# Kernel optimization log

Hardware: AMD Instinct MI355X
Metric: run time of the kernel (lower is better)

Reference implementation:

```python
import jax, jax.numpy as jnp
import numpy as np

K = 10        # neighbors kept (after dropping self)
N_SEEDS = 20  # FPS seeds
H = 0.01      # repulsion bandwidth


def setup_inputs() -> dict:
    key = jax.random.key(0)
    pcs = jax.random.uniform(key, (16, 65536, 3), dtype=jnp.float32)
    return {"pcs": pcs}


def farthest_point_sample(xyz, npoint, key):
    """Iterative FPS. xyz: [B,N,C] -> centroids [B,npoint] (int)."""
    B, N, C = xyz.shape
    distance = jnp.full((B, N), 1e10, dtype=xyz.dtype)
    farthest = jax.random.randint(key, (B,), 0, N)
    bidx = jnp.arange(B)

    def step(carry, _):
        dist_min, far = carry
        centroid = xyz[bidx, far][:, None, :]              # [B,1,C]
        d = jnp.sum((xyz - centroid) ** 2, axis=-1)        # [B,N]
        dist_min = jnp.minimum(dist_min, d)
        return (dist_min, jnp.argmax(dist_min, axis=-1)), far

    _, cents = jax.lax.scan(step, (distance, farthest), None, length=npoint)
    return cents.T  # [B, npoint]


def reference(pcs):
    B, N, C = pcs.shape
    seeds = farthest_point_sample(pcs, N_SEEDS, jax.random.key(1))   # [B,S]
    seeds_value = jnp.take_along_axis(
        pcs, jnp.broadcast_to(seeds[:, :, None], (B, N_SEEDS, C)), axis=1
    )  # [B,S,3]
    diff = pcs[:, :, None, :] - seeds_value[:, None, :, :]           # [B,N,S,3]
    sq = jnp.sum(diff * diff, axis=-1)                               # [B,N,S]
    # safe L2 norm (exact zeros at seed-vs-itself)
    dist = jnp.where(sq == 0, 0.0, jnp.sqrt(jnp.where(sq == 0, 1.0, sq)))
    dist_sn = dist.transpose(0, 2, 1)                                # [B,S,N]
    # k+1 smallest distances per seed, ascending (torch.topk largest=False)
    neg_top, _ = jax.lax.top_k(-dist_sn, K + 1)                      # [B,S,K+1]
    top_dist_net = -neg_top[:, :, 1:]                                # drop self, [B,S,K]
    weights = jnp.exp(-(top_dist_net ** 2) / (H * H))
    repulsion = -top_dist_net * weights
    return repulsion.sum(axis=2).sum(axis=1).mean()
```

## Files before the change

### kernel.cpp

```cpp
#include <hip/hip_runtime.h>
#include <cstdint>
#include <cfloat>
#include <cmath>

#define NPTS 65536
#define NB 16
#define NS 20
#define KK 10
#define FPB 16
#define NSm1 (NS - 1)

struct InitIdx { int idx[NB]; };

static __device__ __forceinline__ unsigned long long
agent_ld(const unsigned long long* p) {
    return __hip_atomic_load(p, __ATOMIC_RELAXED, __HIP_MEMORY_SCOPE_AGENT);
}

__global__ __launch_bounds__(1024) void fps_kernel(const float* __restrict__ pcs,
                                                   int* __restrict__ seeds,
                                                   unsigned long long* __restrict__ fkey,
                                                   InitIdx init) {
    const int u   = blockIdx.x;
    const int xcd = u & 7;
    const int k   = u >> 3;
    const int b   = 2 * xcd + (k >> 4);
    const int j   = k & 15;
    const int t   = threadIdx.x;
    const int lane = t & 63;
    const int w    = t >> 6;
    const float* __restrict__ base = pcs + (size_t)b * NPTS * 3;
    const int pbase = j * 4096 + t * 4;

    const float4* q4 = reinterpret_cast<const float4*>(base + (size_t)pbase * 3);
    float4 A = q4[0], Bv = q4[1], Cv = q4[2];
    float x[4] = { A.x, A.w, Bv.z, Cv.y };
    float y[4] = { A.y, Bv.x, Bv.w, Cv.z };
    float z[4] = { A.z, Bv.y, Cv.x, Cv.w };
    float dm[4] = { 1e10f, 1e10f, 1e10f, 1e10f };

    __shared__ float s_val[16];
    __shared__ int   s_idx[16];
    __shared__ int   s_far;

    int far = init.idx[b];

    for (int s = 0; s < NS; ++s) {
        if (j == 0 && t == 0) seeds[b * NS + s] = far;
        if (s == NSm1) break;

        const float* c = base + (size_t)far * 3;
        const float cx = c[0], cy = c[1], cz = c[2];

        float bestv = -1.0f;
        int   besti = 0;
#pragma unroll
        for (int q = 0; q < 4; ++q) {
            float dx = __fsub_rn(x[q], cx);
            float dy = __fsub_rn(y[q], cy);
            float dz = __fsub_rn(z[q], cz);
            float d  = __fadd_rn(__fadd_rn(__fmul_rn(dx, dx), __fmul_rn(dy, dy)),
                                 __fmul_rn(dz, dz));
            dm[q] = fminf(dm[q], d);
            if (dm[q] > bestv) { bestv = dm[q]; besti = pbase + q; }
        }
#pragma unroll
        for (int off = 32; off >= 1; off >>= 1) {
            float ov = __shfl_down(bestv, off);
            int   oi = __shfl_down(besti, off);
            if (ov > bestv || (ov == bestv && oi < besti)) { bestv = ov; besti = oi; }
        }
        if (lane == 0) { s_val[w] = bestv; s_idx[w] = besti; }
        __syncthreads();

        if (w == 0) {
            unsigned long long kv = 0ULL;
            if (lane < 16) {
                kv = ((unsigned long long)__float_as_uint(s_val[lane]) << 32) |
                     (unsigned long long)(0xFFFFFFFFu - (unsigned int)s_idx[lane]);
            }
#pragma unroll
            for (int off = 8; off >= 1; off >>= 1) {
                unsigned int lo = (unsigned int)kv, hi = (unsigned int)(kv >> 32);
                unsigned int olo = (unsigned int)__shfl_xor((int)lo, off);
                unsigned int ohi = (unsigned int)__shfl_xor((int)hi, off);
                unsigned long long o = ((unsigned long long)ohi << 32) | olo;
                if (o > kv) kv = o;
            }
            unsigned long long* fp = fkey + (size_t)(b * NS + s) * FPB;
            if (lane == 0)
                __hip_atomic_store(&fp[j], kv, __ATOMIC_RELAXED,
                                   __HIP_MEMORY_SCOPE_AGENT);

            const unsigned long long* sl = fp + (lane & 15);
            unsigned long long p0 = agent_ld(sl);
            unsigned long long p1 = agent_ld(sl);
            unsigned long long p2 = agent_ld(sl);
            unsigned long long v;
            for (;;) {
                if (!__any(p0 == 0ULL)) { v = p0; break; }
                p0 = agent_ld(sl);
                if (!__any(p1 == 0ULL)) { v = p1; break; }
                p1 = agent_ld(sl);
                if (!__any(p2 == 0ULL)) { v = p2; break; }
                p2 = agent_ld(sl);
            }
#pragma unroll
            for (int off = 32; off >= 1; off >>= 1) {
                unsigned int lo = (unsigned int)v, hi = (unsigned int)(v >> 32);
                unsigned int olo = (unsigned int)__shfl_xor((int)lo, off);
                unsigned int ohi = (unsigned int)__shfl_xor((int)hi, off);
                unsigned long long o = ((unsigned long long)ohi << 32) | olo;
                if (o > v) v = o;
            }
            if (lane == 0)
                s_far = (int)(0xFFFFFFFFu - (unsigned int)(v & 0xFFFFFFFFull));
        }
        __syncthreads();
        far = s_far;
    }
}

__global__ __launch_bounds__(1024) void knn_kernel(const float* __restrict__ pcs,
                                                   const int* __restrict__ seeds,
                                                   float* __restrict__ out) {
    const int u   = blockIdx.x;
    const int xcd = u & 7;
    const int k   = u >> 3;
    const int b   = 2 * xcd + (k & 1);
    const int s   = k >> 1;
    const int t = threadIdx.x;
    const int lane = t & 63;
    const int w = t >> 6;
    const float* __restrict__ base = pcs + (size_t)b * NPTS * 3;
    const int sidx = seeds[b * NS + s];
    const float cx = base[(size_t)sidx * 3 + 0];
    const float cy = base[(size_t)sidx * 3 + 1];
    const float cz = base[(size_t)sidx * 3 + 2];

    float lst[11];
#pragma unroll
    for (int jj = 0; jj < 11; ++jj) lst[jj] = FLT_MAX;

    for (int i = 0; i < 16; ++i) {
        const int pbase = i * 4096 + t * 4;
        const float4* q4 = reinterpret_cast<const float4*>(base + (size_t)pbase * 3);
        float4 A = q4[0], Bv = q4[1], Cv = q4[2];
        float px[4] = { A.x, A.w, Bv.z, Cv.y };
        float py[4] = { A.y, Bv.x, Bv.w, Cv.z };
        float pz[4] = { A.z, Bv.y, Cv.x, Cv.w };
#pragma unroll
        for (int q = 0; q < 4; ++q) {
            float dx = __fsub_rn(px[q], cx);
            float dy = __fsub_rn(py[q], cy);
            float dz = __fsub_rn(pz[q], cz);
            float sq = __fadd_rn(__fadd_rn(__fmul_rn(dx, dx), __fmul_rn(dy, dy)),
                                 __fmul_rn(dz, dz));
#pragma unroll
            for (int jj = 10; jj >= 1; --jj)
                lst[jj] = __builtin_amdgcn_fmed3f(lst[jj - 1], lst[jj], sq);
            lst[0] = fminf(lst[0], sq);
        }
    }

    __shared__ float s_top[16][11];
    for (int r = 0; r < 11; ++r) {
        float v = lst[0];
#pragma unroll
        for (int off = 32; off >= 1; off >>= 1) v = fminf(v, __shfl_xor(v, off));
        unsigned long long m = __ballot(lst[0] == v);
        if (lane == (int)__ffsll(m) - 1) {
#pragma unroll
            for (int jj = 0; jj < 10; ++jj) lst[jj] = lst[jj + 1];
            lst[10] = FLT_MAX;
        }
        if (lane == 0) s_top[w][r] = v;
    }
    __syncthreads();

    if (w == 0) {
        const float* flat = &s_top[0][0];
        float a0 = flat[lane];
        float a1 = flat[lane + 64];
        float a2 = (lane + 128 < 176) ? flat[lane + 128] : FLT_MAX;

        const float HH = (float)(0.01 * 0.01);
        float acc = 0.0f;
#pragma unroll
        for (int r = 0; r < 11; ++r) {
            float mymin = fminf(a0, fminf(a1, a2));
            float v = mymin;
#pragma unroll
            for (int off = 32; off >= 1; off >>= 1) v = fminf(v, __shfl_xor(v, off));
            unsigned long long m = __ballot(mymin == v);
            if (lane == (int)__ffsll(m) - 1) {
                if (a0 == v)      a0 = FLT_MAX;
                else if (a1 == v) a1 = FLT_MAX;
                else              a2 = FLT_MAX;
            }
            if (lane == 0 && r >= 1) {
                float sq = v;
                float d  = (sq == 0.0f) ? 0.0f : __fsqrt_rn(sq);
                float q2 = __fmul_rn(d, d);
                float wt = expf(__fdiv_rn(-q2, HH));
                acc = __fadd_rn(acc, -__fmul_rn(d, wt));
            }
        }
        if (lane == 0) atomicAdd(out, acc * 0.0625f);
    }
}

static inline uint32_t rotl32(uint32_t x, uint32_t d) { return (x << d) | (x >> (32 - d)); }

static void tf2x32(uint32_t k0, uint32_t k1, uint32_t x0, uint32_t x1,
                   uint32_t& y0, uint32_t& y1) {
    const uint32_t ks[3] = { k0, k1, k0 ^ k1 ^ 0x1BD11BDAu };
    const uint32_t rotA[4] = { 13, 15, 26, 6 };
    const uint32_t rotB[4] = { 17, 29, 16, 24 };
    uint32_t v0 = x0 + ks[0], v1 = x1 + ks[1];
    for (int i = 0; i < 5; ++i) {
        const uint32_t* rot = (i % 2 == 0) ? rotA : rotB;
        for (int j = 0; j < 4; ++j) {
            v0 += v1;
            v1 = rotl32(v1, rot[j]);
            v1 ^= v0;
        }
        v0 += ks[(i + 1) % 3];
        v1 += ks[(i + 2) % 3] + (uint32_t)(i + 1);
    }
    y0 = v0; y1 = v1;
}

extern "C" void kernel_launch(void* const* d_in, const int* in_sizes, int n_in,
                              void* d_out, int out_size, void* d_ws, size_t ws_size,
                              hipStream_t stream) {
    const float* pcs = (const float*)d_in[0];
    float* out = (float*)d_out;

    int* seeds               = (int*)d_ws;
    unsigned long long* fkey = (unsigned long long*)((char*)d_ws + 2048);

    uint32_t k2_0, k2_1;
    tf2x32(0u, 1u, 0u, 1u, k2_0, k2_1);
    InitIdx init;
    for (int i = 0; i < NB; ++i) {
        uint32_t y0, y1;
        tf2x32(k2_0, k2_1, 0u, (uint32_t)i, y0, y1);
        init.idx[i] = (int)((y0 ^ y1) & 0xFFFFu);
    }

    hipMemsetAsync(d_ws, 0, 43008, stream);
    hipMemsetAsync(d_out, 0, sizeof(float), stream);

    hipLaunchKernelGGL(fps_kernel, dim3(NB * FPB), dim3(1024), 0, stream,
                       pcs, seeds, fkey, init);
    hipLaunchKernelGGL(knn_kernel, dim3(NB * NS), dim3(1024), 0, stream,
                       pcs, seeds, out);
}
```

Measured before the change: 82.35 us.

## Halve FPS blocks per batch and split KNN scan into smaller blocks with merge kernel

```diff
diff --git a/kernel.cpp b/kernel.cpp
--- a/kernel.cpp
+++ b/kernel.cpp
@@ -7,7 +7,8 @@
 #define NB 16
 #define NS 20
 #define KK 10
-#define FPB 16
+#define FPB 8
+#define PPT 8
 #define NSm1 (NS - 1)
 
 struct InitIdx { int idx[NB]; };
@@ -24,20 +25,28 @@
     const int u   = blockIdx.x;
     const int xcd = u & 7;
     const int k   = u >> 3;
-    const int b   = 2 * xcd + (k >> 4);
-    const int j   = k & 15;
+    const int b   = 2 * xcd + (k >> 3);
+    const int j   = k & 7;
     const int t   = threadIdx.x;
     const int lane = t & 63;
     const int w    = t >> 6;
     const float* __restrict__ base = pcs + (size_t)b * NPTS * 3;
-    const int pbase = j * 4096 + t * 4;
-
-    const float4* q4 = reinterpret_cast<const float4*>(base + (size_t)pbase * 3);
-    float4 A = q4[0], Bv = q4[1], Cv = q4[2];
-    float x[4] = { A.x, A.w, Bv.z, Cv.y };
-    float y[4] = { A.y, Bv.x, Bv.w, Cv.z };
-    float z[4] = { A.z, Bv.y, Cv.x, Cv.w };
-    float dm[4] = { 1e10f, 1e10f, 1e10f, 1e10f };
+    const int pbase = j * 8192 + t * 8;
+
+    float x[PPT], y[PPT], z[PPT], dm[PPT];
+    {
+        const float4* q4 = reinterpret_cast<const float4*>(base + (size_t)pbase * 3);
+#pragma unroll
+        for (int g = 0; g < 2; ++g) {
+            float4 A = q4[g * 3 + 0], Bv = q4[g * 3 + 1], Cv = q4[g * 3 + 2];
+            x[g*4+0] = A.x;  y[g*4+0] = A.y;  z[g*4+0] = A.z;
+            x[g*4+1] = A.w;  y[g*4+1] = Bv.x; z[g*4+1] = Bv.y;
+            x[g*4+2] = Bv.z; y[g*4+2] = Bv.w; z[g*4+2] = Cv.x;
+            x[g*4+3] = Cv.y; y[g*4+3] = Cv.z; z[g*4+3] = Cv.w;
+        }
+#pragma unroll
+        for (int q = 0; q < PPT; ++q) dm[q] = 1e10f;
+    }
 
     __shared__ float s_val[16];
     __shared__ int   s_idx[16];
@@ -55,7 +64,7 @@
         float bestv = -1.0f;
         int   besti = 0;
 #pragma unroll
-        for (int q = 0; q < 4; ++q) {
+        for (int q = 0; q < PPT; ++q) {
             float dx = __fsub_rn(x[q], cx);
             float dy = __fsub_rn(y[q], cy);
             float dz = __fsub_rn(z[q], cz);
@@ -92,7 +101,7 @@
                 __hip_atomic_store(&fp[j], kv, __ATOMIC_RELAXED,
                                    __HIP_MEMORY_SCOPE_AGENT);
 
-            const unsigned long long* sl = fp + (lane & 15);
+            const unsigned long long* sl = fp + (lane & 7);
             unsigned long long p0 = agent_ld(sl);
             unsigned long long p1 = agent_ld(sl);
             unsigned long long p2 = agent_ld(sl);
@@ -121,14 +130,16 @@
     }
 }
 
-__global__ __launch_bounds__(1024) void knn_kernel(const float* __restrict__ pcs,
-                                                   const int* __restrict__ seeds,
-                                                   float* __restrict__ out) {
+__global__ __launch_bounds__(256) void knn_scan(const float* __restrict__ pcs,
+                                                const int* __restrict__ seeds,
+                                                float* __restrict__ part) {
     const int u   = blockIdx.x;
     const int xcd = u & 7;
     const int k   = u >> 3;
-    const int b   = 2 * xcd + (k & 1);
-    const int s   = k >> 1;
+    const int b   = 2 * xcd + (k / 80);
+    const int rem = k % 80;
+    const int s   = rem >> 2;
+    const int c   = rem & 3;
     const int t = threadIdx.x;
     const int lane = t & 63;
     const int w = t >> 6;
@@ -143,7 +154,7 @@
     for (int jj = 0; jj < 11; ++jj) lst[jj] = FLT_MAX;
 
     for (int i = 0; i < 16; ++i) {
-        const int pbase = i * 4096 + t * 4;
+        const int pbase = c * 16384 + i * 1024 + t * 4;
         const float4* q4 = reinterpret_cast<const float4*>(base + (size_t)pbase * 3);
         float4 A = q4[0], Bv = q4[1], Cv = q4[2];
         float px[4] = { A.x, A.w, Bv.z, Cv.y };
@@ -163,7 +174,7 @@
         }
     }
 
-    __shared__ float s_top[16][11];
+    float* pr = part + ((size_t)((b * NS + s) * 4 + c) * 4 + w) * 11;
     for (int r = 0; r < 11; ++r) {
         float v = lst[0];
 #pragma unroll
@@ -174,40 +185,42 @@
             for (int jj = 0; jj < 10; ++jj) lst[jj] = lst[jj + 1];
             lst[10] = FLT_MAX;
         }
-        if (lane == 0) s_top[w][r] = v;
-    }
-    __syncthreads();
-
-    if (w == 0) {
-        const float* flat = &s_top[0][0];
-        float a0 = flat[lane];
-        float a1 = flat[lane + 64];
-        float a2 = (lane + 128 < 176) ? flat[lane + 128] : FLT_MAX;
-
-        const float HH = (float)(0.01 * 0.01);
-        float acc = 0.0f;
-#pragma unroll
-        for (int r = 0; r < 11; ++r) {
-            float mymin = fminf(a0, fminf(a1, a2));
-            float v = mymin;
-#pragma unroll
-            for (int off = 32; off >= 1; off >>= 1) v = fminf(v, __shfl_xor(v, off));
-            unsigned long long m = __ballot(mymin == v);
-            if (lane == (int)__ffsll(m) - 1) {
-                if (a0 == v)      a0 = FLT_MAX;
-                else if (a1 == v) a1 = FLT_MAX;
-                else              a2 = FLT_MAX;
-            }
-            if (lane == 0 && r >= 1) {
-                float sq = v;
-                float d  = (sq == 0.0f) ? 0.0f : __fsqrt_rn(sq);
-                float q2 = __fmul_rn(d, d);
-                float wt = expf(__fdiv_rn(-q2, HH));
-                acc = __fadd_rn(acc, -__fmul_rn(d, wt));
-            }
-        }
-        if (lane == 0) atomicAdd(out, acc * 0.0625f);
-    }
+        if (lane == 0) pr[r] = v;
+    }
+}
+
+__global__ __launch_bounds__(64) void knn_merge(const float* __restrict__ part,
+                                                float* __restrict__ out) {
+    const int pair = blockIdx.x;
+    const int lane = threadIdx.x;
+    const float* flat = part + (size_t)pair * 176;
+    float a0 = flat[lane];
+    float a1 = flat[lane + 64];
+    float a2 = (lane + 128 < 176) ? flat[lane + 128] : FLT_MAX;
+
+    const float HH = (float)(0.01 * 0.01);
+    float acc = 0.0f;
+#pragma unroll
+    for (int r = 0; r < 11; ++r) {
+        float mymin = fminf(a0, fminf(a1, a2));
+        float v = mymin;
+#pragma unroll
+        for (int off = 32; off >= 1; off >>= 1) v = fminf(v, __shfl_xor(v, off));
+        unsigned long long m = __ballot(mymin == v);
+        if (lane == (int)__ffsll(m) - 1) {
+            if (a0 == v)      a0 = FLT_MAX;
+            else if (a1 == v) a1 = FLT_MAX;
+            else              a2 = FLT_MAX;
+        }
+        if (lane == 0 && r >= 1) {
+            float sq = v;
+            float d  = (sq == 0.0f) ? 0.0f : __fsqrt_rn(sq);
+            float q2 = __fmul_rn(d, d);
+            float wt = expf(__fdiv_rn(-q2, HH));
+            acc = __fadd_rn(acc, -__fmul_rn(d, wt));
+        }
+    }
+    if (lane == 0) atomicAdd(out, acc * 0.0625f);
 }
 
 static inline uint32_t rotl32(uint32_t x, uint32_t d) { return (x << d) | (x >> (32 - d)); }
@@ -239,6 +252,7 @@
 
     int* seeds               = (int*)d_ws;
     unsigned long long* fkey = (unsigned long long*)((char*)d_ws + 2048);
+    float* part              = (float*)((char*)d_ws + 24576);
 
     uint32_t k2_0, k2_1;
     tf2x32(0u, 1u, 0u, 1u, k2_0, k2_1);
@@ -249,11 +263,13 @@
         init.idx[i] = (int)((y0 ^ y1) & 0xFFFFu);
     }
 
-    hipMemsetAsync(d_ws, 0, 43008, stream);
+    hipMemsetAsync(d_ws, 0, 22528, stream);
     hipMemsetAsync(d_out, 0, sizeof(float), stream);
 
     hipLaunchKernelGGL(fps_kernel, dim3(NB * FPB), dim3(1024), 0, stream,
                        pcs, seeds, fkey, init);
-    hipLaunchKernelGGL(knn_kernel, dim3(NB * NS), dim3(1024), 0, stream,
-                       pcs, seeds, out);
-}
+    hipLaunchKernelGGL(knn_scan, dim3(1280), dim3(256), 0, stream,
+                       pcs, seeds, part);
+    hipLaunchKernelGGL(knn_merge, dim3(320), dim3(64), 0, stream,
+                       part, out);
+}
```

After: 81.83 us. Within noise of the previous version (-0.6%).

## Split kNN into chunked multi-seed scan and separate merge kernel

Applied to the files above, without the earlier changes.

```diff
diff --git a/kernel.cpp b/kernel.cpp
--- a/kernel.cpp
+++ b/kernel.cpp
@@ -9,6 +9,9 @@
 #define KK 10
 #define FPB 16
 #define NSm1 (NS - 1)
+#define NCH 8
+#define NSG 4
+#define SPG 5
 
 struct InitIdx { int idx[NB]; };
 
@@ -121,29 +124,38 @@
     }
 }
 
-__global__ __launch_bounds__(1024) void knn_kernel(const float* __restrict__ pcs,
-                                                   const int* __restrict__ seeds,
-                                                   float* __restrict__ out) {
+__global__ __launch_bounds__(256) void knn_scan(const float* __restrict__ pcs,
+                                                const int* __restrict__ seeds,
+                                                float* __restrict__ part) {
     const int u   = blockIdx.x;
     const int xcd = u & 7;
     const int k   = u >> 3;
-    const int b   = 2 * xcd + (k & 1);
-    const int s   = k >> 1;
+    const int b   = 2 * xcd + (k >> 5);
+    const int rem = k & 31;
+    const int ch  = rem >> 2;
+    const int sg  = rem & 3;
     const int t = threadIdx.x;
     const int lane = t & 63;
     const int w = t >> 6;
     const float* __restrict__ base = pcs + (size_t)b * NPTS * 3;
-    const int sidx = seeds[b * NS + s];
-    const float cx = base[(size_t)sidx * 3 + 0];
-    const float cy = base[(size_t)sidx * 3 + 1];
-    const float cz = base[(size_t)sidx * 3 + 2];
-
-    float lst[11];
-#pragma unroll
-    for (int jj = 0; jj < 11; ++jj) lst[jj] = FLT_MAX;
-
-    for (int i = 0; i < 16; ++i) {
-        const int pbase = i * 4096 + t * 4;
+
+    float scx[SPG], scy[SPG], scz[SPG];
+#pragma unroll
+    for (int g = 0; g < SPG; ++g) {
+        const int sidx = seeds[b * NS + sg * SPG + g];
+        scx[g] = base[(size_t)sidx * 3 + 0];
+        scy[g] = base[(size_t)sidx * 3 + 1];
+        scz[g] = base[(size_t)sidx * 3 + 2];
+    }
+
+    float lst[SPG][11];
+#pragma unroll
+    for (int g = 0; g < SPG; ++g)
+#pragma unroll
+        for (int jj = 0; jj < 11; ++jj) lst[g][jj] = FLT_MAX;
+
+    for (int i = 0; i < 8; ++i) {
+        const int pbase = ch * 8192 + i * 1024 + t * 4;
         const float4* q4 = reinterpret_cast<const float4*>(base + (size_t)pbase * 3);
         float4 A = q4[0], Bv = q4[1], Cv = q4[2];
         float px[4] = { A.x, A.w, Bv.z, Cv.y };
@@ -151,63 +163,80 @@
         float pz[4] = { A.z, Bv.y, Cv.x, Cv.w };
 #pragma unroll
         for (int q = 0; q < 4; ++q) {
-            float dx = __fsub_rn(px[q], cx);
-            float dy = __fsub_rn(py[q], cy);
-            float dz = __fsub_rn(pz[q], cz);
-            float sq = __fadd_rn(__fadd_rn(__fmul_rn(dx, dx), __fmul_rn(dy, dy)),
-                                 __fmul_rn(dz, dz));
-#pragma unroll
-            for (int jj = 10; jj >= 1; --jj)
-                lst[jj] = __builtin_amdgcn_fmed3f(lst[jj - 1], lst[jj], sq);
-            lst[0] = fminf(lst[0], sq);
-        }
-    }
-
-    __shared__ float s_top[16][11];
+#pragma unroll
+            for (int g = 0; g < SPG; ++g) {
+                float dx = __fsub_rn(px[q], scx[g]);
+                float dy = __fsub_rn(py[q], scy[g]);
+                float dz = __fsub_rn(pz[q], scz[g]);
+                float sq = __fadd_rn(__fadd_rn(__fmul_rn(dx, dx),
+                                               __fmul_rn(dy, dy)),
+                                     __fmul_rn(dz, dz));
+#pragma unroll
+                for (int jj = 10; jj >= 1; --jj)
+                    lst[g][jj] = __builtin_amdgcn_fmed3f(lst[g][jj - 1],
+                                                         lst[g][jj], sq);
+                lst[g][0] = fminf(lst[g][0], sq);
+            }
+        }
+    }
+
+#pragma unroll
+    for (int g = 0; g < SPG; ++g) {
+        const int s = sg * SPG + g;
+        float* pr = part + ((size_t)(b * NS + s) * NCH * 4 + ch * 4 + w) * 11;
+        for (int r = 0; r < 11; ++r) {
+            float v = lst[g][0];
+#pragma unroll
+            for (int off = 32; off >= 1; off >>= 1) v = fminf(v, __shfl_xor(v, off));
+            unsigned long long m = __ballot(lst[g][0] == v);
+            if (lane == (int)__ffsll(m) - 1) {
+#pragma unroll
+                for (int jj = 0; jj < 10; ++jj) lst[g][jj] = lst[g][jj + 1];
+                lst[g][10] = FLT_MAX;
+            }
+            if (lane == 0) pr[r] = v;
+        }
+    }
+}
+
+__global__ __launch_bounds__(64) void knn_merge(const float* __restrict__ part,
+                                               float* __restrict__ out) {
+    const int pair = blockIdx.x;
+    const int lane = threadIdx.x;
+    const float* flat = part + (size_t)pair * 352;
+    float a0 = flat[lane];
+    float a1 = flat[lane + 64];
+    float a2 = flat[lane + 128];
+    float a3 = flat[lane + 192];
+    float a4 = flat[lane + 256];
+    float a5 = (lane < 32) ? flat[lane + 320] : FLT_MAX;
+
+    const float HH = (float)(0.01 * 0.01);
+    float acc = 0.0f;
+#pragma unroll
     for (int r = 0; r < 11; ++r) {
-        float v = lst[0];
+        float mymin = fminf(fminf(fminf(a0, a1), fminf(a2, a3)), fminf(a4, a5));
+        float v = mymin;
 #pragma unroll
         for (int off = 32; off >= 1; off >>= 1) v = fminf(v, __shfl_xor(v, off));
-        unsigned long long m = __ballot(lst[0] == v);
+        unsigned long long m = __ballot(mymin == v);
         if (lane == (int)__ffsll(m) - 1) {
-#pragma unroll
-            for (int jj = 0; jj < 10; ++jj) lst[jj] = lst[jj + 1];
-            lst[10] = FLT_MAX;
-        }
-        if (lane == 0) s_top[w][r] = v;
-    }
-    __syncthreads();
-
-    if (w == 0) {
-        const float* flat = &s_top[0][0];
-        float a0 = flat[lane];
-        float a1 = flat[lane + 64];
-        float a2 = (lane + 128 < 176) ? flat[lane + 128] : FLT_MAX;
-
-        const float HH = (float)(0.01 * 0.01);
-        float acc = 0.0f;
-#pragma unroll
-        for (int r = 0; r < 11; ++r) {
-            float mymin = fminf(a0, fminf(a1, a2));
-            float v = mymin;
-#pragma unroll
-            for (int off = 32; off >= 1; off >>= 1) v = fminf(v, __shfl_xor(v, off));
-            unsigned long long m = __ballot(mymin == v);
-            if (lane == (int)__ffsll(m) - 1) {
-                if (a0 == v)      a0 = FLT_MAX;
-                else if (a1 == v) a1 = FLT_MAX;
-                else              a2 = FLT_MAX;
-            }
-            if (lane == 0 && r >= 1) {
-                float sq = v;
-                float d  = (sq == 0.0f) ? 0.0f : __fsqrt_rn(sq);
-                float q2 = __fmul_rn(d, d);
-                float wt = expf(__fdiv_rn(-q2, HH));
-                acc = __fadd_rn(acc, -__fmul_rn(d, wt));
-            }
-        }
-        if (lane == 0) atomicAdd(out, acc * 0.0625f);
-    }
+            if (a0 == v)      a0 = FLT_MAX;
+            else if (a1 == v) a1 = FLT_MAX;
+            else if (a2 == v) a2 = FLT_MAX;
+            else if (a3 == v) a3 = FLT_MAX;
+            else if (a4 == v) a4 = FLT_MAX;
+            else              a5 = FLT_MAX;
+        }
+        if (lane == 0 && r >= 1) {
+            float sq = v;
+            float d  = (sq == 0.0f) ? 0.0f : __fsqrt_rn(sq);
+            float q2 = __fmul_rn(d, d);
+            float wt = expf(__fdiv_rn(-q2, HH));
+            acc = __fadd_rn(acc, -__fmul_rn(d, wt));
+        }
+    }
+    if (lane == 0) atomicAdd(out, acc * 0.0625f);
 }
 
 static inline uint32_t rotl32(uint32_t x, uint32_t d) { return (x << d) | (x >> (32 - d)); }
@@ -239,6 +268,7 @@
 
     int* seeds               = (int*)d_ws;
     unsigned long long* fkey = (unsigned long long*)((char*)d_ws + 2048);
+    float* part              = (float*)((char*)d_ws + 49152);
 
     uint32_t k2_0, k2_1;
     tf2x32(0u, 1u, 0u, 1u, k2_0, k2_1);
@@ -254,6 +284,8 @@
 
     hipLaunchKernelGGL(fps_kernel, dim3(NB * FPB), dim3(1024), 0, stream,
                        pcs, seeds, fkey, init);
-    hipLaunchKernelGGL(knn_kernel, dim3(NB * NS), dim3(1024), 0, stream,
-                       pcs, seeds, out);
-}
+    hipLaunchKernelGGL(knn_scan, dim3(512), dim3(256), 0, stream,
+                       pcs, seeds, part);
+    hipLaunchKernelGGL(knn_merge, dim3(320), dim3(64), 0, stream,
+                       part, out);
+}
```

After: 88.15 us. +7.0%, slower.

## Split KNN scan into chunks with sampled threshold filtering and separate merge

Applied to the files above, without the earlier changes.

```diff
diff --git a/kernel.cpp b/kernel.cpp
--- a/kernel.cpp
+++ b/kernel.cpp
@@ -9,6 +9,7 @@
 #define KK 10
 #define FPB 16
 #define NSm1 (NS - 1)
+#define CANDCAP 2048
 
 struct InitIdx { int idx[NB]; };
 
@@ -121,14 +122,39 @@
     }
 }
 
-__global__ __launch_bounds__(1024) void knn_kernel(const float* __restrict__ pcs,
+#define INS11(L, SQ)                                                     \
+    {                                                                    \
+        _Pragma("unroll")                                                \
+        for (int jj = 10; jj >= 1; --jj)                                 \
+            L[jj] = __builtin_amdgcn_fmed3f(L[jj - 1], L[jj], (SQ));     \
+        L[0] = fminf(L[0], (SQ));                                        \
+    }
+
+#define WAVEPOP11(L, DEST)                                               \
+    for (int r = 0; r < 11; ++r) {                                       \
+        float v = L[0];                                                  \
+        _Pragma("unroll")                                                \
+        for (int off = 32; off >= 1; off >>= 1)                          \
+            v = fminf(v, __shfl_xor(v, off));                            \
+        unsigned long long m = __ballot(L[0] == v);                      \
+        if (lane == (int)__ffsll(m) - 1) {                               \
+            _Pragma("unroll")                                            \
+            for (int jj = 0; jj < 10; ++jj) L[jj] = L[jj + 1];           \
+            L[10] = FLT_MAX;                                             \
+        }                                                                \
+        if (lane == 0) (DEST)[r] = v;                                    \
+    }
+
+__global__ __launch_bounds__(256, 4) void knn_scan(const float* __restrict__ pcs,
                                                    const int* __restrict__ seeds,
-                                                   float* __restrict__ out) {
+                                                   float* __restrict__ part) {
     const int u   = blockIdx.x;
     const int xcd = u & 7;
     const int k   = u >> 3;
-    const int b   = 2 * xcd + (k & 1);
-    const int s   = k >> 1;
+    const int b   = 2 * xcd + (k / 80);
+    const int rem = k % 80;
+    const int s   = rem >> 2;
+    const int c   = rem & 3;
     const int t = threadIdx.x;
     const int lane = t & 63;
     const int w = t >> 6;
@@ -138,13 +164,19 @@
     const float cy = base[(size_t)sidx * 3 + 1];
     const float cz = base[(size_t)sidx * 3 + 2];
 
+    __shared__ float s_top[4][11];
+    __shared__ float s_T;
+    __shared__ int   s_cnt;
+    __shared__ float cand[CANDCAP];
+
+    if (t == 0) s_cnt = 0;
+
     float lst[11];
 #pragma unroll
     for (int jj = 0; jj < 11; ++jj) lst[jj] = FLT_MAX;
-
-    for (int i = 0; i < 16; ++i) {
-        const int pbase = i * 4096 + t * 4;
-        const float4* q4 = reinterpret_cast<const float4*>(base + (size_t)pbase * 3);
+    {
+        const int pb = c * 16384 + t * 4;
+        const float4* q4 = reinterpret_cast<const float4*>(base + (size_t)pb * 3);
         float4 A = q4[0], Bv = q4[1], Cv = q4[2];
         float px[4] = { A.x, A.w, Bv.z, Cv.y };
         float py[4] = { A.y, Bv.x, Bv.w, Cv.z };
@@ -156,58 +188,94 @@
             float dz = __fsub_rn(pz[q], cz);
             float sq = __fadd_rn(__fadd_rn(__fmul_rn(dx, dx), __fmul_rn(dy, dy)),
                                  __fmul_rn(dz, dz));
-#pragma unroll
-            for (int jj = 10; jj >= 1; --jj)
-                lst[jj] = __builtin_amdgcn_fmed3f(lst[jj - 1], lst[jj], sq);
-            lst[0] = fminf(lst[0], sq);
-        }
-    }
-
-    __shared__ float s_top[16][11];
-    for (int r = 0; r < 11; ++r) {
-        float v = lst[0];
-#pragma unroll
-        for (int off = 32; off >= 1; off >>= 1) v = fminf(v, __shfl_xor(v, off));
-        unsigned long long m = __ballot(lst[0] == v);
-        if (lane == (int)__ffsll(m) - 1) {
-#pragma unroll
-            for (int jj = 0; jj < 10; ++jj) lst[jj] = lst[jj + 1];
-            lst[10] = FLT_MAX;
-        }
-        if (lane == 0) s_top[w][r] = v;
-    }
+            INS11(lst, sq);
+        }
+    }
+    WAVEPOP11(lst, s_top[w]);
     __syncthreads();
-
     if (w == 0) {
         const float* flat = &s_top[0][0];
-        float a0 = flat[lane];
-        float a1 = flat[lane + 64];
-        float a2 = (lane + 128 < 176) ? flat[lane + 128] : FLT_MAX;
-
-        const float HH = (float)(0.01 * 0.01);
-        float acc = 0.0f;
-#pragma unroll
+        float a = (lane < 44) ? flat[lane] : FLT_MAX;
         for (int r = 0; r < 11; ++r) {
-            float mymin = fminf(a0, fminf(a1, a2));
-            float v = mymin;
+            float v = a;
 #pragma unroll
             for (int off = 32; off >= 1; off >>= 1) v = fminf(v, __shfl_xor(v, off));
-            unsigned long long m = __ballot(mymin == v);
-            if (lane == (int)__ffsll(m) - 1) {
-                if (a0 == v)      a0 = FLT_MAX;
-                else if (a1 == v) a1 = FLT_MAX;
-                else              a2 = FLT_MAX;
-            }
-            if (lane == 0 && r >= 1) {
-                float sq = v;
-                float d  = (sq == 0.0f) ? 0.0f : __fsqrt_rn(sq);
-                float q2 = __fmul_rn(d, d);
-                float wt = expf(__fdiv_rn(-q2, HH));
-                acc = __fadd_rn(acc, -__fmul_rn(d, wt));
-            }
-        }
-        if (lane == 0) atomicAdd(out, acc * 0.0625f);
-    }
+            unsigned long long m = __ballot(a == v);
+            if (lane == (int)__ffsll(m) - 1) a = FLT_MAX;
+            if (r == 10 && lane == 0) s_T = v;
+        }
+    }
+    __syncthreads();
+    const float T = s_T;
+
+    for (int i = 0; i < 16; ++i) {
+        const int pb = c * 16384 + i * 1024 + t * 4;
+        const float4* q4 = reinterpret_cast<const float4*>(base + (size_t)pb * 3);
+        float4 A = q4[0], Bv = q4[1], Cv = q4[2];
+        float px[4] = { A.x, A.w, Bv.z, Cv.y };
+        float py[4] = { A.y, Bv.x, Bv.w, Cv.z };
+        float pz[4] = { A.z, Bv.y, Cv.x, Cv.w };
+#pragma unroll
+        for (int q = 0; q < 4; ++q) {
+            float dx = __fsub_rn(px[q], cx);
+            float dy = __fsub_rn(py[q], cy);
+            float dz = __fsub_rn(pz[q], cz);
+            float sq = __fadd_rn(__fadd_rn(__fmul_rn(dx, dx), __fmul_rn(dy, dy)),
+                                 __fmul_rn(dz, dz));
+            if (sq <= T) {
+                int idx = atomicAdd(&s_cnt, 1);
+                if (idx < CANDCAP) cand[idx] = sq;
+            }
+        }
+    }
+    __syncthreads();
+    const int n = (s_cnt < CANDCAP) ? s_cnt : CANDCAP;
+
+#pragma unroll
+    for (int jj = 0; jj < 11; ++jj) lst[jj] = FLT_MAX;
+    for (int idx = t; idx < n; idx += 256) INS11(lst, cand[idx]);
+    WAVEPOP11(lst, s_top[w]);
+    __syncthreads();
+    if (w == 0) {
+        const float* flat = &s_top[0][0];
+        float a = (lane < 44) ? flat[lane] : FLT_MAX;
+        float* pr = part + (size_t)((b * NS + s) * 4 + c) * 11;
+        for (int r = 0; r < 11; ++r) {
+            float v = a;
+#pragma unroll
+            for (int off = 32; off >= 1; off >>= 1) v = fminf(v, __shfl_xor(v, off));
+            unsigned long long m = __ballot(a == v);
+            if (lane == (int)__ffsll(m) - 1) a = FLT_MAX;
+            if (lane == 0) pr[r] = v;
+        }
+    }
+}
+
+__global__ __launch_bounds__(64) void knn_merge(const float* __restrict__ part,
+                                               float* __restrict__ out) {
+    const int pair = blockIdx.x;
+    const int lane = threadIdx.x;
+    const float* flat = part + (size_t)pair * 44;
+    float a = (lane < 44) ? flat[lane] : FLT_MAX;
+
+    const float HH = (float)(0.01 * 0.01);
+    float acc = 0.0f;
+#pragma unroll
+    for (int r = 0; r < 11; ++r) {
+        float v = a;
+#pragma unroll
+        for (int off = 32; off >= 1; off >>= 1) v = fminf(v, __shfl_xor(v, off));
+        unsigned long long m = __ballot(a == v);
+        if (lane == (int)__ffsll(m) - 1) a = FLT_MAX;
+        if (lane == 0 && r >= 1) {
+            float sq = v;
+            float d  = (sq == 0.0f) ? 0.0f : __fsqrt_rn(sq);
+            float q2 = __fmul_rn(d, d);
+            float wt = expf(__fdiv_rn(-q2, HH));
+            acc = __fadd_rn(acc, -__fmul_rn(d, wt));
+        }
+    }
+    if (lane == 0) atomicAdd(out, acc * 0.0625f);
 }
 
 static inline uint32_t rotl32(uint32_t x, uint32_t d) { return (x << d) | (x >> (32 - d)); }
@@ -239,6 +307,7 @@
 
     int* seeds               = (int*)d_ws;
     unsigned long long* fkey = (unsigned long long*)((char*)d_ws + 2048);
+    float* part              = (float*)((char*)d_ws + 49152);
 
     uint32_t k2_0, k2_1;
     tf2x32(0u, 1u, 0u, 1u, k2_0, k2_1);
@@ -254,6 +323,8 @@
 
     hipLaunchKernelGGL(fps_kernel, dim3(NB * FPB), dim3(1024), 0, stream,
                        pcs, seeds, fkey, init);
-    hipLaunchKernelGGL(knn_kernel, dim3(NB * NS), dim3(1024), 0, stream,
-                       pcs, seeds, out);
-}
+    hipLaunchKernelGGL(knn_scan, dim3(1280), dim3(256), 0, stream,
+                       pcs, seeds, part);
+    hipLaunchKernelGGL(knn_merge, dim3(320), dim3(64), 0, stream,
+                       part, out);
+}
```

After: 86.35 us. 4.9% more time.
